# Kernel optimization log

Hardware: AMD Instinct MI355X
Metric: run time of the kernel (lower is better)

The kernel has to match this reference:

```python
import jax, jax.numpy as jnp
import numpy as np

B, C, H, W = 8, 192, 56, 56
K = 9          # kernel_size (k nearest neighbors), dilation=1
G = 4          # conv groups in BasicConv
EPS_BN = 1e-5


def setup_inputs() -> dict:
    key = jax.random.key(0)
    ks = jax.random.split(key, 5)
    C2 = 2 * C
    gi = C2 // G
    x = jax.random.normal(ks[0], (B, C, H, W), jnp.float32)
    # fc1: Conv2d(C,C,1) + BN(C)
    w_fc1 = jax.random.normal(ks[1], (C, C), jnp.float32) * (1.0 / np.sqrt(C))
    b_fc1 = jnp.zeros((C,), jnp.float32)
    g_fc1 = jnp.ones((C,), jnp.float32)
    be_fc1 = jnp.zeros((C,), jnp.float32)
    # graph conv BasicConv: grouped Conv2d(2C,2C,1,groups=4) + BN(2C) + GELU
    w_gc = jax.random.normal(ks[2], (C2, gi), jnp.float32) * np.sqrt(2.0 / gi)  # kaiming
    b_gc = jnp.zeros((C2,), jnp.float32)
    g_gc = jnp.ones((C2,), jnp.float32)
    be_gc = jnp.zeros((C2,), jnp.float32)
    # fc2: Conv2d(2C,C,1) + BN(C)
    w_fc2 = jax.random.normal(ks[3], (C, C2), jnp.float32) * (1.0 / np.sqrt(C2))
    b_fc2 = jnp.zeros((C,), jnp.float32)
    g_fc2 = jnp.ones((C,), jnp.float32)
    be_fc2 = jnp.zeros((C,), jnp.float32)
    return dict(x=x, w_fc1=w_fc1, b_fc1=b_fc1, g_fc1=g_fc1, be_fc1=be_fc1,
                w_gc=w_gc, b_gc=b_gc, g_gc=g_gc, be_gc=be_gc,
                w_fc2=w_fc2, b_fc2=b_fc2, g_fc2=g_fc2, be_fc2=be_fc2)


def _bn(x, g, b):
    # training-mode BatchNorm over (batch, points) per channel; x: [B,N,C]
    mu = jnp.mean(x, axis=(0, 1))
    var = jnp.var(x, axis=(0, 1))  # biased, as torch BN uses for normalization
    return (x - mu) * jax.lax.rsqrt(var + EPS_BN) * g + b


def _forward(x, w_fc1, b_fc1, g_fc1, be_fc1, w_gc, b_gc, g_gc, be_gc,
             w_fc2, b_fc2, g_fc2, be_fc2):
    Bb, Cc, Hh, Ww = x.shape
    N = Hh * Ww
    x0 = x.reshape(Bb, Cc, N).transpose(0, 2, 1)          # [B,N,C]
    h = _bn(x0 @ w_fc1.T + b_fc1, g_fc1, be_fc1)          # fc1

    # --- dynamic kNN graph on L2-normalized features (no-grad in torch) ---
    f = jax.lax.stop_gradient(h)
    f = f / jnp.maximum(jnp.linalg.norm(f, axis=-1, keepdims=True), 1e-12)
    sq = jnp.sum(f * f, axis=-1, keepdims=True)           # [B,N,1]
    dist = sq - 2.0 * jnp.einsum('bnc,bmc->bnm', f, f) + sq.transpose(0, 2, 1)
    _, idx = jax.lax.top_k(-dist, K)                      # [B,N,K] neighbor indices

    # --- max-relative aggregation ---
    xj = h[jnp.arange(Bb)[:, None, None], idx]            # gather: [B,N,K,C]
    rel = jnp.max(xj - h[:, :, None, :], axis=2)          # [B,N,C]
    # interleave channels: c*2 + {0: h, 1: rel} (matches cat(dim=2).reshape)
    feat = jnp.stack([h, rel], axis=-1).reshape(Bb, N, 2 * Cc)

    # --- grouped 1x1 conv + BN + GELU ---
    C2 = 2 * Cc
    gi = C2 // G
    fg = feat.reshape(Bb, N, G, gi)
    wg = w_gc.reshape(G, gi, gi)                          # [group, out_pg, in_pg]
    y = jnp.einsum('bngi,goi->bngo', fg, wg).reshape(Bb, N, C2) + b_gc
    y = jax.nn.gelu(_bn(y, g_gc, be_gc), approximate=False)

    # --- fc2 + residual ---
    out = _bn(y @ w_fc2.T + b_fc2, g_fc2, be_fc2) + x0
    return out.transpose(0, 2, 1).reshape(Bb, Cc, Hh, Ww)


def reference(x, w_fc1, b_fc1, g_fc1, be_fc1, w_gc, b_gc, g_gc, be_gc,
              w_fc2, b_fc2, g_fc2, be_fc2):
    return _forward(x, w_fc1, b_fc1, g_fc1, be_fc1, w_gc, b_gc, g_gc, be_gc,
                    w_fc2, b_fc2, g_fc2, be_fc2)
```

## Files before the change

### kernel.cpp

```cpp
#include <hip/hip_runtime.h>
#include <math.h>

#define BB 8
#define CC 192
#define NN 3136
#define NR 25088
#define C2 384
#define GI 96
#define KNN 9
#define NCHUNK 256
#define RPC 98
#define EPS_BN 1e-5f

typedef unsigned short ushortT;
typedef unsigned int uintT;
typedef _Float16 f16x8 __attribute__((ext_vector_type(8)));
typedef float f32x4 __attribute__((ext_vector_type(4)));

static __device__ __forceinline__ ushortT f16b(_Float16 v) {
  union { _Float16 f; ushortT u; } x; x.f = v; return x.u;
}
static __device__ __forceinline__ float f16tof(ushortT u) {
  union { ushortT u; _Float16 f; } x; x.u = u; return (float)x.f;
}
static __device__ __forceinline__ float packdi(float d, int cidx) {
  return __uint_as_float((__float_as_uint(d) & 0xFFFFF800u) | (uintT)cidx);
}
static __device__ __forceinline__ void split8(const float* vv, f16x8& hi, f16x8& lo) {
  #pragma unroll
  for (int e = 0; e < 8; ++e) {
    _Float16 hh = (_Float16)vv[e];
    hi[e] = hh;
    lo[e] = (_Float16)((vv[e] - (float)hh)*4096.f);
  }
}

__global__ __launch_bounds__(256) void k_fc1(const float* __restrict__ x,
        const float* __restrict__ w1, const float* __restrict__ b1,
        float* __restrict__ z) {
  __shared__ __align__(16) float Xs[32*68];
  __shared__ __align__(16) float Ws[32*68];
  int b = blockIdx.z, n0 = blockIdx.x*64, c0 = blockIdx.y*64;
  int tid = threadIdx.x;
  int tcol = tid & 15, trow = tid >> 4;
  float acc[4][4] = {};
  const float4* xf4 = (const float4*)x;
  const float4* wf4 = (const float4*)w1;
  for (int kb = 0; kb < 6; ++kb) {
    int k0 = kb*32;
    __syncthreads();
    #pragma unroll
    for (int s = 0; s < 2; ++s) {
      int q = tid + 256*s;
      int kk = q >> 4, nq = q & 15;
      ((float4*)Xs)[kk*17 + nq] = xf4[(size_t)(b*CC + k0 + kk)*784 + (n0>>2) + nq];
    }
    #pragma unroll
    for (int s = 0; s < 2; ++s) {
      int q = tid + 256*s;
      int cc = q >> 3, kq = q & 7;
      float4 v = wf4[(size_t)(c0 + cc)*48 + (k0>>2) + kq];
      Ws[(kq*4+0)*68 + cc] = v.x;
      Ws[(kq*4+1)*68 + cc] = v.y;
      Ws[(kq*4+2)*68 + cc] = v.z;
      Ws[(kq*4+3)*68 + cc] = v.w;
    }
    __syncthreads();
    #pragma unroll 8
    for (int kk = 0; kk < 32; ++kk) {
      float4 a4 = ((const float4*)Xs)[kk*17 + trow];
      float4 b4 = ((const float4*)Ws)[kk*17 + tcol];
      float av[4] = {a4.x,a4.y,a4.z,a4.w};
      float bv[4] = {b4.x,b4.y,b4.z,b4.w};
      #pragma unroll
      for (int i = 0; i < 4; ++i)
        #pragma unroll
        for (int j = 0; j < 4; ++j)
          acc[i][j] += av[i]*bv[j];
    }
  }
  float4 bias = ((const float4*)b1)[(c0>>2) + tcol];
  float bb4[4] = {bias.x,bias.y,bias.z,bias.w};
  #pragma unroll
  for (int i = 0; i < 4; ++i) {
    int n = n0 + trow*4 + i;
    float4 o;
    o.x = acc[i][0] + bb4[0]; o.y = acc[i][1] + bb4[1];
    o.z = acc[i][2] + bb4[2]; o.w = acc[i][3] + bb4[3];
    ((float4*)z)[(size_t)(b*NN + n)*48 + (c0>>2) + tcol] = o;
  }
}

__global__ void k_stats_part(const float* __restrict__ src, int C, float* __restrict__ part) {
  int c = threadIdx.x;
  int chunk = blockIdx.x;
  float s = 0.f, ss = 0.f;
  const float* p = src + (size_t)chunk*RPC*C + c;
  for (int r = 0; r < RPC; ++r) {
    float v = p[(size_t)r*C];
    s += v; ss += v*v;
  }
  part[(size_t)chunk*C + c] = s;
  part[(size_t)(NCHUNK + chunk)*C + c] = ss;
}

__global__ __launch_bounds__(256) void k_stats_fin(const float* __restrict__ part, int C,
      const float* __restrict__ g, const float* __restrict__ be,
      float* __restrict__ scale, float* __restrict__ shift) {
  int c = blockIdx.x;
  int t = threadIdx.x;
  float s  = part[(size_t)t*C + c];
  float ss = part[(size_t)(NCHUNK + t)*C + c];
  #pragma unroll
  for (int o = 32; o; o >>= 1) { s += __shfl_xor(s, o); ss += __shfl_xor(ss, o); }
  __shared__ float sred[4], ssred[4];
  int w = t >> 6, lane = t & 63;
  if (lane == 0) { sred[w] = s; ssred[w] = ss; }
  __syncthreads();
  if (t == 0) {
    float s2  = (sred[0] + sred[1]) + (sred[2] + sred[3]);
    float ss2 = (ssred[0] + ssred[1]) + (ssred[2] + ssred[3]);
    float mu = s2 / (float)NR;
    float var = ss2/(float)NR - mu*mu;
    float rs = 1.0f / sqrtf(var + EPS_BN);
    float sc = g[c]*rs;
    scale[c] = sc;
    shift[c] = be[c] - mu*sc;
  }
}

__global__ void k_packw(const float* __restrict__ src, int n4,
                        ushortT* __restrict__ hi, ushortT* __restrict__ lo) {
  int i = blockIdx.x*256 + threadIdx.x;
  if (i >= n4) return;
  float4 v = ((const float4*)src)[i];
  float vv[4] = {v.x, v.y, v.z, v.w};
  ushortT hb[4], lb[4];
  #pragma unroll
  for (int t = 0; t < 4; ++t) {
    _Float16 hh = (_Float16)vv[t];
    float r = vv[t] - (float)hh;
    _Float16 ll = (_Float16)(r*4096.f);
    hb[t] = f16b(hh); lb[t] = f16b(ll);
  }
  ((uint2*)hi)[i] = make_uint2((uintT)hb[0] | ((uintT)hb[1]<<16), (uintT)hb[2] | ((uintT)hb[3]<<16));
  ((uint2*)lo)[i] = make_uint2((uintT)lb[0] | ((uintT)lb[1]<<16), (uintT)lb[2] | ((uintT)lb[3]<<16));
}

__global__ __launch_bounds__(256) void k_h_f(float* __restrict__ h,
      ushortT* __restrict__ fhi, ushortT* __restrict__ flo, float* __restrict__ sqh,
      const float* __restrict__ scale, const float* __restrict__ shift) {
  __shared__ __align__(16) float fbuf[4][192];
  int w = threadIdx.x >> 6, lane = threadIdx.x & 63;
  size_t row = (size_t)blockIdx.x*4 + w;
  float* hp = h + row*CC;
  float hv[3]; float s = 0.f;
  #pragma unroll
  for (int t = 0; t < 3; ++t) {
    int c = lane + 64*t;
    float v = hp[c]*scale[c] + shift[c];
    hv[t] = v; s += v*v;
  }
  #pragma unroll
  for (int o = 32; o; o >>= 1) s += __shfl_xor(s, o);
  float eta = fmaxf(sqrtf(s), 1e-12f);
  float fv[3]; float s2 = 0.f;
  #pragma unroll
  for (int t = 0; t < 3; ++t) { fv[t] = hv[t]/eta; s2 += fv[t]*fv[t]; }
  #pragma unroll
  for (int o = 32; o; o >>= 1) s2 += __shfl_xor(s2, o);
  #pragma unroll
  for (int t = 0; t < 3; ++t) {
    int c = lane + 64*t;
    hp[c] = hv[t];
    fbuf[w][c] = fv[t];
  }
  if (lane == 0) sqh[row] = 0.5f*s2;
  __syncthreads();
  if (threadIdx.x < 192) {
    int r = threadIdx.x / 48, q = threadIdx.x % 48;
    size_t grow = (size_t)blockIdx.x*4 + r;
    float4 v = *(float4*)&fbuf[r][q*4];
    _Float16 a0=(_Float16)v.x, a1=(_Float16)v.y, a2=(_Float16)v.z, a3=(_Float16)v.w;
    float r0=v.x-(float)a0, r1=v.y-(float)a1, r2=v.z-(float)a2, r3=v.w-(float)a3;
    _Float16 b0=(_Float16)(r0*4096.f), b1=(_Float16)(r1*4096.f);
    _Float16 b2=(_Float16)(r2*4096.f), b3=(_Float16)(r3*4096.f);
    uintT hi0 = (uintT)f16b(a0) | ((uintT)f16b(a1)<<16);
    uintT hi1 = (uintT)f16b(a2) | ((uintT)f16b(a3)<<16);
    uintT lo0 = (uintT)f16b(b0) | ((uintT)f16b(b1)<<16);
    uintT lo1 = (uintT)f16b(b2) | ((uintT)f16b(b3)<<16);
    ((uint2*)(fhi + grow*CC))[q] = make_uint2(hi0, hi1);
    ((uint2*)(flo + grow*CC))[q] = make_uint2(lo0, lo1);
  }
}

__global__ __launch_bounds__(256) void k_knn12(const ushortT* __restrict__ fhi_,
    const float* __restrict__ sqh, int* __restrict__ idx12) {
  __shared__ __align__(16) f16x8 AHs[2][768];
  __shared__ float sqs[1568];
  int id = blockIdx.x;
  int b = id & 7, half = (id >> 3) & 1, rt = id >> 4;
  int tid = threadIdx.x, w = tid >> 6, lane = tid & 63;
  int l15 = lane & 15, kg = lane >> 4;

  const f16x8* FH = (const f16x8*)(fhi_ + (size_t)b*NN*CC);
  int cbase = half*1568;
  const f16x8* FC = FH + (size_t)cbase*24;

  int soff[3];
  #pragma unroll
  for (int i = 0; i < 3; ++i) {
    int s = i*256 + tid;
    int rr = s/24, u = s - rr*24;
    soff[i] = rr*24 + (u ^ (rr&7));
  }
  #pragma unroll
  for (int i = 0; i < 3; ++i)
    __builtin_amdgcn_global_load_lds(
      (const __attribute__((address_space(1))) void*)(FC + soff[i]),
      (__attribute__((address_space(3))) void*)&AHs[0][i*256 + w*64], 16, 0, 0);

  for (int i = tid; i < 1568/4; i += 256)
    ((float4*)sqs)[i] = ((const float4*)(sqh + (size_t)b*NN + cbase))[i];

  int row = rt*64 + w*16 + l15;
  f16x8 Bh[6];
  #pragma unroll
  for (int ks = 0; ks < 6; ++ks)
    Bh[ks] = FH[(size_t)row*24 + ks*4 + kg];

  float PD[12];
  #pragma unroll
  for (int t = 0; t < 12; ++t) PD[t] = -3.0e38f;

  __syncthreads();

  int buf = 0;
  for (int ct = 0; ct < 49; ++ct) {
    if (ct + 1 < 49) {
      #pragma unroll
      for (int i = 0; i < 3; ++i)
        __builtin_amdgcn_global_load_lds(
          (const __attribute__((address_space(1))) void*)(FC + (ct+1)*768 + soff[i]),
          (__attribute__((address_space(3))) void*)&AHs[buf^1][i*256 + w*64], 16, 0, 0);
    }
    f32x4 acc0 = {0.f,0.f,0.f,0.f}, acc1 = {0.f,0.f,0.f,0.f};
    #pragma unroll
    for (int ks = 0; ks < 6; ++ks) {
      int ub = ks*4 + kg;
      f16x8 a0 = AHs[buf][(     l15)*24 + (ub ^ (l15&7))];
      f16x8 a1 = AHs[buf][(16 + l15)*24 + (ub ^ (l15&7))];
      acc0 = __builtin_amdgcn_mfma_f32_16x16x32_f16(a0, Bh[ks], acc0, 0, 0, 0);
      acc1 = __builtin_amdgcn_mfma_f32_16x16x32_f16(a1, Bh[ks], acc1, 0, 0, 0);
    }
    int jbl = ct*32 + kg*4;
    float4 s0 = *(float4*)&sqs[jbl];
    float4 s1 = *(float4*)&sqs[jbl + 16];
    float S[8] = {acc0[0]-s0.x, acc0[1]-s0.y, acc0[2]-s0.z, acc0[3]-s0.w,
                  acc1[0]-s1.x, acc1[1]-s1.y, acc1[2]-s1.z, acc1[3]-s1.w};
    #pragma unroll
    for (int r = 0; r < 8; ++r)
      S[r] = packdi(S[r], jbl + (r&3) + ((r>>2)<<4));
#define CED(i,j) { float hi_ = fmaxf(S[i],S[j]), lo_ = fminf(S[i],S[j]); S[i]=hi_; S[j]=lo_; }
    CED(0,1) CED(2,3) CED(4,5) CED(6,7)
    CED(0,2) CED(1,3) CED(4,6) CED(5,7)
    CED(1,2) CED(5,6)
    CED(0,4) CED(1,5) CED(2,6) CED(3,7)
    CED(2,4) CED(3,5)
    CED(1,2) CED(3,4) CED(5,6)
#undef CED
    #pragma unroll
    for (int i = 0; i < 8; ++i) PD[i] = fmaxf(PD[i], S[i]);
#define CEA(i,j) { float lo_ = fminf(PD[i],PD[j]), hi_ = fmaxf(PD[i],PD[j]); PD[i]=lo_; PD[j]=hi_; }
    CEA(0,8) CEA(1,9) CEA(2,10) CEA(3,11)
    CEA(0,4) CEA(1,5) CEA(2,6) CEA(3,7)
    CEA(0,2) CEA(1,3) CEA(4,6) CEA(5,7) CEA(8,10) CEA(9,11)
    CEA(0,1) CEA(2,3) CEA(4,5) CEA(6,7) CEA(8,9) CEA(10,11)
#undef CEA
    __syncthreads();
    buf ^= 1;
  }

  #pragma unroll
  for (int t = 0; t < 12; ++t) {
    float od = __shfl_xor(PD[t], 32);
    float od2 = (kg < 2) ? od : -3.0e38f;
    PD[0] = fmaxf(PD[0], od2);
    #pragma unroll
    for (int t2 = 0; t2 < 11; ++t2) {
      float a = PD[t2], c2 = PD[t2+1];
      PD[t2] = fminf(a, c2); PD[t2+1] = fmaxf(a, c2);
    }
  }
  #pragma unroll
  for (int t = 0; t < 12; ++t) {
    float od = __shfl_xor(PD[t], 16);
    float od2 = (kg == 0) ? od : -3.0e38f;
    PD[0] = fmaxf(PD[0], od2);
    #pragma unroll
    for (int t2 = 0; t2 < 11; ++t2) {
      float a = PD[t2], c2 = PD[t2+1];
      PD[t2] = fminf(a, c2); PD[t2+1] = fmaxf(a, c2);
    }
  }
  if (kg == 0) {
    size_t base = ((size_t)(b*NN + row)*2 + half)*12;
    #pragma unroll
    for (int t = 0; t < 12; ++t)
      idx12[base + t] = cbase + (int)(__float_as_uint(PD[t]) & 0x7FFu);
  }
}

__global__ __launch_bounds__(256) void k_refine(const ushortT* __restrict__ fhi_,
    const ushortT* __restrict__ flo_, const float* __restrict__ sqh,
    const int* __restrict__ idx12, int* __restrict__ idxg) {
  int id = blockIdx.x;
  int b = id & 7, rq = id >> 3;
  int w = threadIdx.x >> 6, lane = threadIdx.x & 63;
  int row = rq*4 + w;
  const ushortT* FHb = fhi_ + (size_t)b*NN*CC;
  const ushortT* FLb = flo_ + (size_t)b*NN*CC;
  float rv[3];
  #pragma unroll
  for (int t = 0; t < 3; ++t) {
    int c = lane + 64*t;
    rv[t] = f16tof(FHb[(size_t)row*CC + c]) + f16tof(FLb[(size_t)row*CC + c])*2.44140625e-4f;
  }
  const int* JP = idx12 + (size_t)(b*NN + row)*24;
  float TD[9]; int TI[9];
  #pragma unroll
  for (int t = 0; t < 9; ++t) { TD[t] = -3.0e38f; TI[t] = 0x7fffffff; }
  #pragma unroll
  for (int g = 0; g < 4; ++g) {
    int J6[6]; float s6[6];
    #pragma unroll
    for (int e = 0; e < 6; ++e) J6[e] = JP[g*6 + e];
    #pragma unroll
    for (int e = 0; e < 6; ++e) {
      int j = J6[e];
      float s = 0.f;
      #pragma unroll
      for (int t = 0; t < 3; ++t) {
        int c = lane + 64*t;
        float cv = f16tof(FHb[(size_t)j*CC + c]) + f16tof(FLb[(size_t)j*CC + c])*2.44140625e-4f;
        s = fmaf(rv[t], cv, s);
      }
      s6[e] = s;
    }
    #pragma unroll
    for (int o = 32; o; o >>= 1) {
      #pragma unroll
      for (int e = 0; e < 6; ++e) s6[e] += __shfl_xor(s6[e], o);
    }
    #pragma unroll
    for (int e = 0; e < 6; ++e) {
      int j = J6[e];
      float d = s6[e] - sqh[(size_t)b*NN + j];
      bool ins = (d > TD[0]) || (d == TD[0] && j < TI[0]);
      if (ins) {
        TD[0] = d; TI[0] = j;
        #pragma unroll
        for (int t = 0; t < 8; ++t) {
          bool sw = (TD[t] > TD[t+1]) || (TD[t] == TD[t+1] && TI[t] < TI[t+1]);
          if (sw) {
            float td = TD[t]; TD[t] = TD[t+1]; TD[t+1] = td;
            int ti = TI[t]; TI[t] = TI[t+1]; TI[t+1] = ti;
          }
        }
      }
    }
  }
  if (lane == 0) {
    size_t base = (size_t)(b*NN + row)*KNN;
    #pragma unroll
    for (int t = 0; t < KNN; ++t) idxg[base + t] = TI[t];
  }
}

__global__ __launch_bounds__(256) void k_gather(const float* __restrict__ h,
    const int* __restrict__ idxg, float* __restrict__ feat) {
  int w = threadIdx.x >> 6, lane = threadIdx.x & 63;
  size_t rg = (size_t)blockIdx.x*4 + w;
  int b = (int)(rg / NN);
  int n = (int)(rg % NN);
  const float* hb = h + (size_t)b*NN*CC;
  int j[KNN];
  #pragma unroll
  for (int t = 0; t < KNN; ++t) j[t] = idxg[rg*KNN + t];
  float2* featp = (float2*)feat;
  #pragma unroll
  for (int t = 0; t < 3; ++t) {
    int c = lane + 64*t;
    float self = hb[(size_t)n*CC + c];
    float m = -3.0e38f;
    #pragma unroll
    for (int k = 0; k < KNN; ++k) m = fmaxf(m, hb[(size_t)j[k]*CC + c]);
    featp[rg*CC + c] = make_float2(self, m - self);
  }
}

__global__ __launch_bounds__(256) void k_gconv(float* __restrict__ feat,
    const ushortT* __restrict__ wgh, const ushortT* __restrict__ wgl,
    const float* __restrict__ bgc, float* __restrict__ y) {
  int rt = blockIdx.x, g = blockIdx.y;
  int tid = threadIdx.x, w = tid >> 6, lane = tid & 63;
  int l15 = lane & 15, kg = lane >> 4;
  int row = rt*64 + w*16 + l15;
  const float4* F4 = (const float4*)feat;
  const f16x8* AH  = (const f16x8*)wgh;
  const f16x8* AL  = (const f16x8*)wgl;
  f16x8 Bh[3], Bl[3];
  #pragma unroll
  for (int ks = 0; ks < 3; ++ks) {
    float4 v0 = F4[(size_t)row*96 + g*24 + ks*8 + kg*2];
    float4 v1 = F4[(size_t)row*96 + g*24 + ks*8 + kg*2 + 1];
    float vv[8] = {v0.x,v0.y,v0.z,v0.w,v1.x,v1.y,v1.z,v1.w};
    split8(vv, Bh[ks], Bl[ks]);
  }
  #pragma unroll 3
  for (int nt = 0; nt < 6; ++nt) {
    f32x4 hh = {0.f,0.f,0.f,0.f}, hl = {0.f,0.f,0.f,0.f}, lh = {0.f,0.f,0.f,0.f};
    #pragma unroll
    for (int ks = 0; ks < 3; ++ks) {
      size_t au = (size_t)(g*GI + nt*16 + l15)*12 + ks*4 + kg;
      f16x8 Ah = AH[au], Al = AL[au];
      hh = __builtin_amdgcn_mfma_f32_16x16x32_f16(Ah, Bh[ks], hh, 0, 0, 0);
      hl = __builtin_amdgcn_mfma_f32_16x16x32_f16(Ah, Bl[ks], hl, 0, 0, 0);
      lh = __builtin_amdgcn_mfma_f32_16x16x32_f16(Al, Bh[ks], lh, 0, 0, 0);
    }
    float4 bias = ((const float4*)bgc)[g*24 + nt*4 + kg];
    float bb[4] = {bias.x, bias.y, bias.z, bias.w};
    float ov[4];
    #pragma unroll
    for (int r = 0; r < 4; ++r)
      ov[r] = fmaf(hl[r] + lh[r], 2.44140625e-4f, hh[r]) + bb[r];
    float4 o; o.x = ov[0]; o.y = ov[1]; o.z = ov[2]; o.w = ov[3];
    ((float4*)y)[(size_t)row*96 + g*24 + nt*4 + kg] = o;
  }
}

__global__ void k_bn_gelu(const float* __restrict__ y, ushortT* __restrict__ y2hi,
    ushortT* __restrict__ y2lo, const float* __restrict__ scale,
    const float* __restrict__ shift) {
  size_t i = (size_t)blockIdx.x*blockDim.x + threadIdx.x;
  float4 v = ((const float4*)y)[i];
  int c4 = (int)(i % 96);
  float4 sc = ((const float4*)scale)[c4], sh = ((const float4*)shift)[c4];
  float vv[4] = {v.x*sc.x+sh.x, v.y*sc.y+sh.y, v.z*sc.z+sh.z, v.w*sc.w+sh.w};
  ushortT hb[4], lb[4];
  #pragma unroll
  for (int t = 0; t < 4; ++t) {
    float g = 0.5f*vv[t]*(1.0f + erff(vv[t]*0.70710678118654752440f));
    _Float16 hh = (_Float16)g;
    float r = g - (float)hh;
    hb[t] = f16b(hh); lb[t] = f16b((_Float16)(r*4096.f));
  }
  ((uint2*)y2hi)[i] = make_uint2((uintT)hb[0] | ((uintT)hb[1]<<16), (uintT)hb[2] | ((uintT)hb[3]<<16));
  ((uint2*)y2lo)[i] = make_uint2((uintT)lb[0] | ((uintT)lb[1]<<16), (uintT)lb[2] | ((uintT)lb[3]<<16));
}

__global__ __launch_bounds__(256) void k_fc2(const ushortT* __restrict__ y2hi,
    const ushortT* __restrict__ y2lo, const ushortT* __restrict__ w2h,
    const ushortT* __restrict__ w2l, const float* __restrict__ b2, float* __restrict__ op) {
  int rt = blockIdx.x;
  int tid = threadIdx.x, w = tid >> 6, lane = tid & 63;
  int l15 = lane & 15, kg = lane >> 4;
  int row = rt*64 + w*16 + l15;
  const f16x8* YH = (const f16x8*)y2hi;
  const f16x8* YL = (const f16x8*)y2lo;
  const f16x8* AH = (const f16x8*)w2h;
  const f16x8* AL = (const f16x8*)w2l;
  f16x8 Bh[12], Bl[12];
  #pragma unroll
  for (int ks = 0; ks < 12; ++ks) {
    size_t u = (size_t)row*48 + ks*4 + kg;
    Bh[ks] = YH[u]; Bl[ks] = YL[u];
  }
  #pragma unroll 4
  for (int nt = 0; nt < 12; ++nt) {
    f32x4 hh = {0.f,0.f,0.f,0.f}, hl = {0.f,0.f,0.f,0.f}, lh = {0.f,0.f,0.f,0.f};
    #pragma unroll
    for (int ks = 0; ks < 12; ++ks) {
      size_t au = (size_t)(nt*16 + l15)*48 + ks*4 + kg;
      f16x8 Ah = AH[au], Al = AL[au];
      hh = __builtin_amdgcn_mfma_f32_16x16x32_f16(Ah, Bh[ks], hh, 0, 0, 0);
      hl = __builtin_amdgcn_mfma_f32_16x16x32_f16(Ah, Bl[ks], hl, 0, 0, 0);
      lh = __builtin_amdgcn_mfma_f32_16x16x32_f16(Al, Bh[ks], lh, 0, 0, 0);
    }
    float4 bias = ((const float4*)b2)[nt*4 + kg];
    float bb[4] = {bias.x, bias.y, bias.z, bias.w};
    float ov[4];
    #pragma unroll
    for (int r = 0; r < 4; ++r)
      ov[r] = fmaf(hl[r] + lh[r], 2.44140625e-4f, hh[r]) + bb[r];
    float4 o; o.x = ov[0]; o.y = ov[1]; o.z = ov[2]; o.w = ov[3];
    ((float4*)op)[(size_t)row*48 + nt*4 + kg] = o;
  }
}

__global__ __launch_bounds__(256) void k_final(const float* __restrict__ op,
    const float* __restrict__ x, const float* __restrict__ scale,
    const float* __restrict__ shift, float* __restrict__ out) {
  __shared__ float t[32][33];
  int n0 = blockIdx.x*32, c0 = blockIdx.y*32, b = blockIdx.z;
  int tx = threadIdx.x, ty = threadIdx.y;
  #pragma unroll
  for (int s = 0; s < 4; ++s) {
    int r = ty + 8*s;
    int c = c0 + tx;
    t[r][tx] = op[((size_t)b*NN + n0 + r)*CC + c]*scale[c] + shift[c];
  }
  __syncthreads();
  #pragma unroll
  for (int s = 0; s < 4; ++s) {
    int c = ty + 8*s;
    size_t o = ((size_t)b*CC + c0 + c)*NN + n0 + tx;
    out[o] = t[tx][c] + x[o];
  }
}

extern "C" void kernel_launch(void* const* d_in, const int* in_sizes, int n_in,
                              void* d_out, int out_size, void* d_ws, size_t ws_size,
                              hipStream_t stream) {
  (void)in_sizes; (void)n_in; (void)out_size; (void)ws_size;
  const float* x   = (const float*)d_in[0];
  const float* w1  = (const float*)d_in[1];
  const float* b1  = (const float*)d_in[2];
  const float* g1  = (const float*)d_in[3];
  const float* be1 = (const float*)d_in[4];
  const float* wgc = (const float*)d_in[5];
  const float* bgc = (const float*)d_in[6];
  const float* g2  = (const float*)d_in[7];
  const float* be2 = (const float*)d_in[8];
  const float* w2  = (const float*)d_in[9];
  const float* b2  = (const float*)d_in[10];
  const float* g3  = (const float*)d_in[11];
  const float* be3 = (const float*)d_in[12];
  float* ws = (float*)d_ws;

  float* h      = ws;
  ushortT* fhi  = (ushortT*)(ws + 4816896);
  ushortT* flo  = (ushortT*)(ws + 7225344);
  float* feat   = ws + 4816896;
  float* y      = feat;
  ushortT* y2hi = (ushortT*)ws;
  ushortT* y2lo = (ushortT*)(ws + 14450688);
  float* op     = ws + 4816896;
  float* sqh    = ws + 14450688;
  int*   idxg   = (int*)(ws + 14475776);
  int*   idx12  = (int*)(ws + 14701568);
  float* st     = ws + 19267584;
  float* part   = ws + 19269120;
  ushortT* w2h  = (ushortT*)(ws + 19465728);
  ushortT* w2l  = (ushortT*)(ws + 19502592);
  ushortT* wgh  = (ushortT*)(ws + 19539456);
  ushortT* wgl  = (ushortT*)(ws + 19557888);
  float* sc1 = st;        float* sh1 = st + 192;
  float* sc2 = st + 384;  float* sh2 = st + 768;
  float* sc3 = st + 1152; float* sh3 = st + 1344;
  float* out = (float*)d_out;

  k_packw<<<72, 256, 0, stream>>>(w2, 18432, w2h, w2l);
  k_packw<<<36, 256, 0, stream>>>(wgc, 9216, wgh, wgl);
  k_fc1<<<dim3(49,3,8), 256, 0, stream>>>(x, w1, b1, h);
  k_stats_part<<<NCHUNK, CC, 0, stream>>>(h, CC, part);
  k_stats_fin<<<CC, 256, 0, stream>>>(part, CC, g1, be1, sc1, sh1);
  k_h_f<<<NR/4, 256, 0, stream>>>(h, fhi, flo, sqh, sc1, sh1);
  k_knn12<<<dim3(784), 256, 0, stream>>>(fhi, sqh, idx12);
  k_refine<<<dim3(6272), 256, 0, stream>>>(fhi, flo, sqh, idx12, idxg);
  k_gather<<<NR/4, 256, 0, stream>>>(h, idxg, feat);
  k_gconv<<<dim3(392,4), 256, 0, stream>>>(feat, wgh, wgl, bgc, y);
  k_stats_part<<<NCHUNK, C2, 0, stream>>>(y, C2, part);
  k_stats_fin<<<C2, 256, 0, stream>>>(part, C2, g2, be2, sc2, sh2);
  k_bn_gelu<<<9408, 256, 0, stream>>>(y, y2hi, y2lo, sc2, sh2);
  k_fc2<<<392, 256, 0, stream>>>(y2hi, y2lo, w2h, w2l, b2, op);
  k_stats_part<<<NCHUNK, CC, 0, stream>>>(op, CC, part);
  k_stats_fin<<<CC, 256, 0, stream>>>(part, CC, g3, be3, sc3, sh3);
  k_final<<<dim3(98,6,8), dim3(32,8), 0, stream>>>(op, x, sc3, sh3, out);
}
```

Baseline: 420.5 us.

## Vectorize k_refine candidate dot products with 8-lane groups per candidate

The refine kernel previously had all 64 lanes cooperate on each candidate's dot product using scalar 16-bit loads and a full 64-lane shuffle reduction. Now each 8-lane subgroup handles one candidate, using 128-bit vector loads of the hi/lo half-precision rows and a 3-step shuffle reduction. Distances go through shared memory before the serial top-9 insertion. This cuts load instruction count and reduction overhead in exchange for more registers (24 row values plus 24 indices) and a block barrier.

```diff
diff --git a/kernel.cpp b/kernel.cpp
--- a/kernel.cpp
+++ b/kernel.cpp
@@ -314,58 +314,72 @@
 __global__ __launch_bounds__(256) void k_refine(const ushortT* __restrict__ fhi_,
     const ushortT* __restrict__ flo_, const float* __restrict__ sqh,
     const int* __restrict__ idx12, int* __restrict__ idxg) {
+  __shared__ float Ds[4][24];
   int id = blockIdx.x;
   int b = id & 7, rq = id >> 3;
   int w = threadIdx.x >> 6, lane = threadIdx.x & 63;
+  int g8 = lane >> 3, l8 = lane & 7;
   int row = rq*4 + w;
   const ushortT* FHb = fhi_ + (size_t)b*NN*CC;
   const ushortT* FLb = flo_ + (size_t)b*NN*CC;
-  float rv[3];
-  #pragma unroll
-  for (int t = 0; t < 3; ++t) {
-    int c = lane + 64*t;
-    rv[t] = f16tof(FHb[(size_t)row*CC + c]) + f16tof(FLb[(size_t)row*CC + c])*2.44140625e-4f;
+
+  float rv[24];
+  {
+    const uint4* ph = (const uint4*)(FHb + (size_t)row*CC + l8*24);
+    const uint4* pl = (const uint4*)(FLb + (size_t)row*CC + l8*24);
+    #pragma unroll
+    for (int i = 0; i < 3; ++i) {
+      uint4 qh = ph[i], ql = pl[i];
+      f16x8 vh = *(f16x8*)&qh, vl = *(f16x8*)&ql;
+      #pragma unroll
+      for (int e = 0; e < 8; ++e)
+        rv[i*8+e] = (float)vh[e] + (float)vl[e]*2.44140625e-4f;
+    }
   }
   const int* JP = idx12 + (size_t)(b*NN + row)*24;
+  int J[24];
+  #pragma unroll
+  for (int q = 0; q < 24; ++q) J[q] = JP[q];
+
+  #pragma unroll
+  for (int p = 0; p < 3; ++p) {
+    int q = g8 + p*8;
+    int j = J[q];
+    const uint4* ch = (const uint4*)(FHb + (size_t)j*CC + l8*24);
+    const uint4* cl = (const uint4*)(FLb + (size_t)j*CC + l8*24);
+    float s = 0.f;
+    #pragma unroll
+    for (int i = 0; i < 3; ++i) {
+      uint4 qh = ch[i], ql = cl[i];
+      f16x8 vh = *(f16x8*)&qh, vl = *(f16x8*)&ql;
+      #pragma unroll
+      for (int e = 0; e < 8; ++e) {
+        float cv = (float)vh[e] + (float)vl[e]*2.44140625e-4f;
+        s = fmaf(rv[i*8+e], cv, s);
+      }
+    }
+    s += __shfl_xor(s, 1);
+    s += __shfl_xor(s, 2);
+    s += __shfl_xor(s, 4);
+    if (l8 == 0) Ds[w][q] = s - sqh[(size_t)b*NN + j];
+  }
+  __syncthreads();
+
   float TD[9]; int TI[9];
   #pragma unroll
   for (int t = 0; t < 9; ++t) { TD[t] = -3.0e38f; TI[t] = 0x7fffffff; }
   #pragma unroll
-  for (int g = 0; g < 4; ++g) {
-    int J6[6]; float s6[6];
-    #pragma unroll
-    for (int e = 0; e < 6; ++e) J6[e] = JP[g*6 + e];
-    #pragma unroll
-    for (int e = 0; e < 6; ++e) {
-      int j = J6[e];
-      float s = 0.f;
+  for (int q = 0; q < 24; ++q) {
+    float d = Ds[w][q]; int j = J[q];
+    bool ins = (d > TD[0]) || (d == TD[0] && j < TI[0]);
+    if (ins) {
+      TD[0] = d; TI[0] = j;
       #pragma unroll
-      for (int t = 0; t < 3; ++t) {
-        int c = lane + 64*t;
-        float cv = f16tof(FHb[(size_t)j*CC + c]) + f16tof(FLb[(size_t)j*CC + c])*2.44140625e-4f;
-        s = fmaf(rv[t], cv, s);
-      }
-      s6[e] = s;
-    }
-    #pragma unroll
-    for (int o = 32; o; o >>= 1) {
-      #pragma unroll
-      for (int e = 0; e < 6; ++e) s6[e] += __shfl_xor(s6[e], o);
-    }
-    #pragma unroll
-    for (int e = 0; e < 6; ++e) {
-      int j = J6[e];
-      float d = s6[e] - sqh[(size_t)b*NN + j];
-      bool ins = (d > TD[0]) || (d == TD[0] && j < TI[0]);
-      if (ins) {
-        TD[0] = d; TI[0] = j;
-        #pragma unroll
-        for (int t = 0; t < 8; ++t) {
-          bool sw = (TD[t] > TD[t+1]) || (TD[t] == TD[t+1] && TI[t] < TI[t+1]);
-          if (sw) {
-            float td = TD[t]; TD[t] = TD[t+1]; TD[t+1] = td;
-            int ti = TI[t]; TI[t] = TI[t+1]; TI[t+1] = ti;
-          }
+      for (int t = 0; t < 8; ++t) {
+        bool sw = (TD[t] > TD[t+1]) || (TD[t] == TD[t+1] && TI[t] < TI[t+1]);
+        if (sw) {
+          float td = TD[t]; TD[t] = TD[t+1]; TD[t+1] = td;
+          int ti = TI[t]; TI[t] = TI[t+1]; TI[t+1] = ti;
         }
       }
     }
```

After: 431.5 us. 1.03x slower.
